# Optimization experiments

Measured on AMD Instinct MI355X. Metric: run time of the kernel, lower is better.

Reference implementation:

```python
import jax, jax.numpy as jnp
import numpy as np

B, T, I, H = 64, 1024, 512, 1024

def setup_inputs() -> dict:
    key = jax.random.key(0)
    k1, k2, k3 = jax.random.split(key, 3)
    x = jax.random.normal(k1, (B, T, I), dtype=jnp.float32)
    # xavier_uniform for input_w, orthogonal for hidden_w (approx: QR of gaussian)
    limit = float(np.sqrt(6.0 / (I + H)))
    input_w = jax.random.uniform(k2, (I, H), minval=-limit, maxval=limit, dtype=jnp.float32)
    g = jax.random.normal(k3, (H, H), dtype=jnp.float32)
    q, r = jnp.linalg.qr(g)
    hidden_w = q * jnp.sign(jnp.diag(r))[None, :]
    b = jnp.zeros((H,), dtype=jnp.float32)
    return {"x": x, "hidden_w": hidden_w, "input_w": input_w, "b": b}

def reference(x, hidden_w, input_w, b):
    # Precompute input projection in one batched GEMM: [B,T,H]
    xp = jnp.einsum('bti,ih->bth', x, input_w) + b
    h0 = jnp.zeros((x.shape[0], hidden_w.shape[0]), dtype=x.dtype)

    def step(h, xt):  # xt: [B,H]
        h = jnp.tanh(h @ hidden_w + xt)
        return h, h

    _, hs = jax.lax.scan(step, h0, jnp.swapaxes(xp, 0, 1))  # hs: [T,B,H]
    return jnp.swapaxes(hs, 0, 1)  # [B,T,H]
```

## Files before the change

kernel.cpp:

```cpp
#include <hip/hip_runtime.h>

#define B_  64
#define T_  1024
#define I_  512
#define H_  1024

typedef short short8 __attribute__((ext_vector_type(8)));
typedef float f32x4  __attribute__((ext_vector_type(4)));
typedef unsigned int u32x4 __attribute__((ext_vector_type(4)));
typedef unsigned long long u64;

__device__ __forceinline__ unsigned short f2bf(float f) {
    unsigned int u = __float_as_uint(f);
    unsigned int r = u + 0x7fffu + ((u >> 16) & 1u);
    return (unsigned short)(r >> 16);
}
__device__ __forceinline__ float bf2f(unsigned short s) {
    return __uint_as_float(((unsigned int)s) << 16);
}

__device__ __forceinline__ u32x4 load_b128_agent(const void* p) {
    u32x4 r;
    asm volatile("global_load_dwordx4 %0, %1, off sc1"
                 : "=v"(r) : "v"(p) : "memory");
    return r;
}

#define BM 128
#define BN 128
#define BK 8

__global__ __launch_bounds__(256) void proj_kernel(
    const float* __restrict__ x, const float* __restrict__ w,
    const float* __restrict__ bias, float* __restrict__ out)
{
    __shared__ float As[BK][BM];
    __shared__ float Bs[BK][BN];

    const int tid = threadIdx.x;
    const int m0 = blockIdx.y * BM;
    const int n0 = blockIdx.x * BN;
    const int tx = tid & 15;
    const int ty = tid >> 4;

    const int arow = tid >> 1;
    const int acol = (tid & 1) * 4;
    const int brow = tid >> 5;
    const int bcol = (tid & 31) * 4;

    float acc[2][4][2][4];
    #pragma unroll
    for (int a = 0; a < 2; a++)
        #pragma unroll
        for (int b = 0; b < 4; b++)
            #pragma unroll
            for (int c = 0; c < 2; c++)
                #pragma unroll
                for (int d = 0; d < 4; d++) acc[a][b][c][d] = 0.f;

    for (int k0 = 0; k0 < I_; k0 += BK) {
        float4 av = *(const float4*)&x[(size_t)(m0 + arow) * I_ + k0 + acol];
        float4 bv = *(const float4*)&w[(size_t)(k0 + brow) * H_ + n0 + bcol];
        __syncthreads();
        As[acol + 0][arow] = av.x;
        As[acol + 1][arow] = av.y;
        As[acol + 2][arow] = av.z;
        As[acol + 3][arow] = av.w;
        *(float4*)&Bs[brow][bcol] = bv;
        __syncthreads();
        #pragma unroll
        for (int kk = 0; kk < BK; kk++) {
            float4 a0 = *(const float4*)&As[kk][ty * 4];
            float4 a1 = *(const float4*)&As[kk][64 + ty * 4];
            float4 b0 = *(const float4*)&Bs[kk][tx * 4];
            float4 b1 = *(const float4*)&Bs[kk][64 + tx * 4];
            const float am[2][4] = {{a0.x,a0.y,a0.z,a0.w},{a1.x,a1.y,a1.z,a1.w}};
            const float bn[2][4] = {{b0.x,b0.y,b0.z,b0.w},{b1.x,b1.y,b1.z,b1.w}};
            #pragma unroll
            for (int mb = 0; mb < 2; mb++)
                #pragma unroll
                for (int mr = 0; mr < 4; mr++)
                    #pragma unroll
                    for (int nb = 0; nb < 2; nb++)
                        #pragma unroll
                        for (int nr = 0; nr < 4; nr++)
                            acc[mb][mr][nb][nr] += am[mb][mr] * bn[nb][nr];
        }
    }

    float4 bias0 = *(const float4*)&bias[n0 + tx * 4];
    float4 bias1 = *(const float4*)&bias[n0 + 64 + tx * 4];
    const float bb[2][4] = {{bias0.x,bias0.y,bias0.z,bias0.w},
                            {bias1.x,bias1.y,bias1.z,bias1.w}};
    #pragma unroll
    for (int mb = 0; mb < 2; mb++)
        #pragma unroll
        for (int mr = 0; mr < 4; mr++) {
            int m = m0 + mb * 64 + ty * 4 + mr;
            #pragma unroll
            for (int nb = 0; nb < 2; nb++) {
                float4 v;
                v.x = acc[mb][mr][nb][0] + bb[nb][0];
                v.y = acc[mb][mr][nb][1] + bb[nb][1];
                v.z = acc[mb][mr][nb][2] + bb[nb][2];
                v.w = acc[mb][mr][nb][3] + bb[nb][3];
                *(float4*)&out[(size_t)m * H_ + n0 + nb * 64 + tx * 4] = v;
            }
        }
}

#define PFD 8

__global__ __launch_bounds__(256, 1) void scan_kernel(
    const float* __restrict__ W,
    float* __restrict__ out,
    unsigned int* __restrict__ hbuf,
    int* __restrict__ flags)
{
    __shared__ short8 wlds[32][64];

    const int wg   = blockIdx.x;
    const int tid  = threadIdx.x;
    const int wave = tid >> 6;
    const int lane = tid & 63;
    const int quad = lane >> 4;
    const int l16  = lane & 15;
    const int jbase = wg * 16;
    const int b0    = wave * 16;
    const int j     = jbase + l16;

    short8 wh[32];
    #pragma unroll
    for (int kc = 0; kc < 32; kc++) {
        short8 wlv;
        #pragma unroll
        for (int i = 0; i < 8; i++) {
            float wv = W[(size_t)(kc * 32 + quad * 8 + i) * H_ + j];
            unsigned short hi = f2bf(wv);
            wh[kc][i] = (short)hi;
            wlv[i] = (short)f2bf(wv - bf2f(hi));
        }
        if ((kc >> 3) == wave) wlds[kc][lane] = wlv;
    }
    __syncthreads();

    const size_t TH = (size_t)T_ * H_;
    size_t oidx[4];
    float xv[4];
    #pragma unroll
    for (int r = 0; r < 4; r++) {
        int b = b0 + quad * 4 + r;
        oidx[r] = (size_t)b * TH + j;
        xv[r] = out[oidx[r]];
    }

    const char* hb_base = (const char*)hbuf + (size_t)wave * 65536
                        + (size_t)lane * 16;
    const int pbase = ((j >> 5) << 9) + (((j >> 2) & 1) << 8)
                    + ((j >> 3) & 3) * 64 + quad * 16 + (j & 3);
    unsigned int* pb_base = hbuf + (size_t)wave * 16384 + pbase;

    int* flagp = flags + wave * 64;

    for (int t = 0; t < T_; t++) {
        float nxv[4] = {0.f, 0.f, 0.f, 0.f};
        if (t + 1 < T_) {
            #pragma unroll
            for (int r = 0; r < 4; r++) nxv[r] = out[oidx[r] + H_];
        }

        f32x4 a0 = {0.f,0.f,0.f,0.f}, a1 = {0.f,0.f,0.f,0.f},
              a2 = {0.f,0.f,0.f,0.f};
        if (t > 0) {
            while (true) {
                int v = __hip_atomic_load(&flagp[lane], __ATOMIC_RELAXED,
                                          __HIP_MEMORY_SCOPE_AGENT);
                if (__all(v >= t)) break;
            }
            __builtin_amdgcn_fence(__ATOMIC_ACQUIRE, "workgroup");

            const char* hb = hb_base + (size_t)((t - 1) & 1) * 262144;

            u32x4 buf[PFD][2];
            #pragma unroll
            for (int d = 0; d < PFD; d++) {
                buf[d][0] = load_b128_agent(hb + d * 2048);
                buf[d][1] = load_b128_agent(hb + d * 2048 + 1024);
            }

            #pragma unroll
            for (int kc = 0; kc < 32; kc++) {
                if (kc < 24) {
                    asm volatile("s_waitcnt vmcnt(14)" ::: "memory");
                } else if (kc == 24) {
                    asm volatile("s_waitcnt vmcnt(0)" ::: "memory");
                }
                __builtin_amdgcn_sched_barrier(0);

                u32x4 c0 = buf[kc & (PFD - 1)][0];
                u32x4 c1 = buf[kc & (PFD - 1)][1];
                short8 ah, al;
                #pragma unroll
                for (int i = 0; i < 4; i++) {
                    ah[i]     = (short)(c0[i] >> 16);
                    al[i]     = (short)(c0[i] & 0xffffu);
                    ah[4 + i] = (short)(c1[i] >> 16);
                    al[4 + i] = (short)(c1[i] & 0xffffu);
                }
                short8 wlv = wlds[kc][lane];
                a0 = __builtin_amdgcn_mfma_f32_16x16x32_bf16(ah, wh[kc], a0, 0, 0, 0);
                a1 = __builtin_amdgcn_mfma_f32_16x16x32_bf16(ah, wlv,    a1, 0, 0, 0);
                a2 = __builtin_amdgcn_mfma_f32_16x16x32_bf16(al, wh[kc], a2, 0, 0, 0);

                if (kc + PFD < 32) {
                    buf[kc & (PFD - 1)][0] =
                        load_b128_agent(hb + (kc + PFD) * 2048);
                    buf[kc & (PFD - 1)][1] =
                        load_b128_agent(hb + (kc + PFD) * 2048 + 1024);
                }
            }
        }

        float hv[4];
        #pragma unroll
        for (int r = 0; r < 4; r++)
            hv[r] = tanhf(a0[r] + a1[r] + a2[r] + xv[r]);

        if (t + 1 < T_) {
            unsigned int* pb = pb_base + (size_t)(t & 1) * 65536;
            #pragma unroll
            for (int r = 0; r < 4; r++) {
                unsigned short hi = f2bf(hv[r]);
                unsigned short lo = f2bf(hv[r] - bf2f(hi));
                unsigned int pk = ((unsigned int)hi << 16) | (unsigned int)lo;
                __hip_atomic_store(&pb[r * 4], pk, __ATOMIC_RELAXED,
                                   __HIP_MEMORY_SCOPE_AGENT);
            }
            asm volatile("s_waitcnt vmcnt(0)" ::: "memory");
            if (lane == 0)
                __hip_atomic_store(&flagp[wg], t + 1, __ATOMIC_RELAXED,
                                   __HIP_MEMORY_SCOPE_AGENT);
        }

        #pragma unroll
        for (int r = 0; r < 4; r++) {
            out[oidx[r]] = hv[r];
            oidx[r] += H_;
            xv[r] = nxv[r];
        }
    }
}

extern "C" void kernel_launch(void* const* d_in, const int* in_sizes, int n_in,
                              void* d_out, int out_size, void* d_ws, size_t ws_size,
                              hipStream_t stream) {
    const float* x        = (const float*)d_in[0];
    const float* hidden_w = (const float*)d_in[1];
    const float* input_w  = (const float*)d_in[2];
    const float* bias     = (const float*)d_in[3];
    float* out = (float*)d_out;

    unsigned int* hbuf = (unsigned int*)d_ws;
    int* flags = (int*)((char*)d_ws + (size_t)512 * 1024);

    hipMemsetAsync(flags, 0, 4 * 64 * sizeof(int), stream);

    dim3 pgrid(H_ / BN, (B_ * T_) / BM);
    proj_kernel<<<pgrid, 256, 0, stream>>>(x, input_w, bias, out);
    scan_kernel<<<64, 256, 0, stream>>>(hidden_w, out, hbuf, flags);
}
```

Measured before the change: 8.276 ms.

## Halve scan workgroups to 32, each computing 32 hidden columns from LDS weights

The persistent scan kernel now runs 32 workgroups instead of 64, and each one computes two 16-column groups of the hidden state per step. Both the high and low bf16 weight splits now sit in LDS instead of the high split being held in registers. Fewer workgroups means fewer flags to poll in the per-step grid-wide barrier, and a short sleep is added to the spin loop. The cost is twice the MFMA work per workgroup on the serial critical path, plus extra LDS reads each step.

```diff
diff --git a/kernel.cpp b/kernel.cpp
--- a/kernel.cpp
+++ b/kernel.cpp
@@ -110,6 +110,7 @@
 }
 
 #define PFD 8
+#define NWG 32
 
 __global__ __launch_bounds__(256, 1) void scan_kernel(
     const float* __restrict__ W,
@@ -117,7 +118,8 @@
     unsigned int* __restrict__ hbuf,
     int* __restrict__ flags)
 {
-    __shared__ short8 wlds[32][64];
+    __shared__ short8 whds[2][32][64];
+    __shared__ short8 wlds[2][32][64];
 
     const int wg   = blockIdx.x;
     const int tid  = threadIdx.x;
@@ -125,57 +127,78 @@
     const int lane = tid & 63;
     const int quad = lane >> 4;
     const int l16  = lane & 15;
-    const int jbase = wg * 16;
+    const int jbase = wg * 32;
     const int b0    = wave * 16;
-    const int j     = jbase + l16;
-
-    short8 wh[32];
+
     #pragma unroll
     for (int kc = 0; kc < 32; kc++) {
-        short8 wlv;
-        #pragma unroll
-        for (int i = 0; i < 8; i++) {
-            float wv = W[(size_t)(kc * 32 + quad * 8 + i) * H_ + j];
-            unsigned short hi = f2bf(wv);
-            wh[kc][i] = (short)hi;
-            wlv[i] = (short)f2bf(wv - bf2f(hi));
-        }
-        if ((kc >> 3) == wave) wlds[kc][lane] = wlv;
+        if ((kc >> 3) == wave) {
+            #pragma unroll
+            for (int g = 0; g < 2; g++) {
+                const int j = jbase + g * 16 + l16;
+                short8 whv, wlv;
+                #pragma unroll
+                for (int i = 0; i < 8; i++) {
+                    float wv = W[(size_t)(kc * 32 + quad * 8 + i) * H_ + j];
+                    unsigned short hi = f2bf(wv);
+                    whv[i] = (short)hi;
+                    wlv[i] = (short)f2bf(wv - bf2f(hi));
+                }
+                whds[g][kc][lane] = whv;
+                wlds[g][kc][lane] = wlv;
+            }
+        }
     }
     __syncthreads();
 
     const size_t TH = (size_t)T_ * H_;
     size_t oidx[4];
-    float xv[4];
+    float xv[2][4];
     #pragma unroll
     for (int r = 0; r < 4; r++) {
         int b = b0 + quad * 4 + r;
-        oidx[r] = (size_t)b * TH + j;
-        xv[r] = out[oidx[r]];
+        oidx[r] = (size_t)b * TH + jbase + l16;
+        xv[0][r] = out[oidx[r]];
+        xv[1][r] = out[oidx[r] + 16];
     }
 
     const char* hb_base = (const char*)hbuf + (size_t)wave * 65536
                         + (size_t)lane * 16;
-    const int pbase = ((j >> 5) << 9) + (((j >> 2) & 1) << 8)
-                    + ((j >> 3) & 3) * 64 + quad * 16 + (j & 3);
-    unsigned int* pb_base = hbuf + (size_t)wave * 16384 + pbase;
-
-    int* flagp = flags + wave * 64;
+    unsigned int* pb_base[2];
+    #pragma unroll
+    for (int g = 0; g < 2; g++) {
+        const int pj = jbase + g * 16 + l16;
+        const int pbase = ((pj >> 5) << 9) + (((pj >> 2) & 1) << 8)
+                        + ((pj >> 3) & 3) * 64 + quad * 16 + (pj & 3);
+        pb_base[g] = hbuf + (size_t)wave * 16384 + pbase;
+    }
+
+    int* flagp = flags + wave * NWG;
 
     for (int t = 0; t < T_; t++) {
-        float nxv[4] = {0.f, 0.f, 0.f, 0.f};
+        float nxv[2][4] = {{0.f,0.f,0.f,0.f},{0.f,0.f,0.f,0.f}};
         if (t + 1 < T_) {
             #pragma unroll
-            for (int r = 0; r < 4; r++) nxv[r] = out[oidx[r] + H_];
-        }
-
-        f32x4 a0 = {0.f,0.f,0.f,0.f}, a1 = {0.f,0.f,0.f,0.f},
-              a2 = {0.f,0.f,0.f,0.f};
+            for (int r = 0; r < 4; r++) {
+                nxv[0][r] = out[oidx[r] + H_];
+                nxv[1][r] = out[oidx[r] + H_ + 16];
+            }
+        }
+
+        f32x4 acc[2][3];
+        #pragma unroll
+        for (int g = 0; g < 2; g++)
+            #pragma unroll
+            for (int s = 0; s < 3; s++)
+                acc[g][s] = (f32x4){0.f, 0.f, 0.f, 0.f};
+
         if (t > 0) {
             while (true) {
-                int v = __hip_atomic_load(&flagp[lane], __ATOMIC_RELAXED,
+                int v = __hip_atomic_load(&flagp[lane & (NWG - 1)],
+                                          __ATOMIC_RELAXED,
                                           __HIP_MEMORY_SCOPE_AGENT);
                 if (__all(v >= t)) break;
+                __builtin_amdgcn_s_sleep(1);
             }
             __builtin_amdgcn_fence(__ATOMIC_ACQUIRE, "workgroup");
 
@@ -207,10 +230,16 @@
                     ah[4 + i] = (short)(c1[i] >> 16);
                     al[4 + i] = (short)(c1[i] & 0xffffu);
                 }
-                short8 wlv = wlds[kc][lane];
-                a0 = __builtin_amdgcn_mfma_f32_16x16x32_bf16(ah, wh[kc], a0, 0, 0, 0);
-                a1 = __builtin_amdgcn_mfma_f32_16x16x32_bf16(ah, wlv,    a1, 0, 0, 0);
-                a2 = __builtin_amdgcn_mfma_f32_16x16x32_bf16(al, wh[kc], a2, 0, 0, 0);
+                short8 wh0 = whds[0][kc][lane];
+                short8 wl0 = wlds[0][kc][lane];
+                short8 wh1 = whds[1][kc][lane];
+                short8 wl1 = wlds[1][kc][lane];
+                acc[0][0] = __builtin_amdgcn_mfma_f32_16x16x32_bf16(ah, wh0, acc[0][0], 0, 0, 0);
+                acc[0][1] = __builtin_amdgcn_mfma_f32_16x16x32_bf16(ah, wl0, acc[0][1], 0, 0, 0);
+                acc[0][2] = __builtin_amdgcn_mfma_f32_16x16x32_bf16(al, wh0, acc[0][2], 0, 0, 0);
+                acc[1][0] = __builtin_amdgcn_mfma_f32_16x16x32_bf16(ah, wh1, acc[1][0], 0, 0, 0);
+                acc[1][1] = __builtin_amdgcn_mfma_f32_16x16x32_bf16(ah, wl1, acc[1][1], 0, 0, 0);
+                acc[1][2] = __builtin_amdgcn_mfma_f32_16x16x32_bf16(al, wh1, acc[1][2], 0, 0, 0);
 
                 if (kc + PFD < 32) {
                     buf[kc & (PFD - 1)][0] =
@@ -221,20 +250,27 @@
             }
         }
 
-        float hv[4];
-        #pragma unroll
-        for (int r = 0; r < 4; r++)
-            hv[r] = tanhf(a0[r] + a1[r] + a2[r] + xv[r]);
+        float hv[2][4];
+        #pragma unroll
+        for (int g = 0; g < 2; g++)
+            #pragma unroll
+            for (int r = 0; r < 4; r++)
+                hv[g][r] = tanhf(acc[g][0][r] + acc[g][1][r] + acc[g][2][r]
+                                 + xv[g][r]);
 
         if (t + 1 < T_) {
-            unsigned int* pb = pb_base + (size_t)(t & 1) * 65536;
-            #pragma unroll
-            for (int r = 0; r < 4; r++) {
-                unsigned short hi = f2bf(hv[r]);
-                unsigned short lo = f2bf(hv[r] - bf2f(hi));
-                unsigned int pk = ((unsigned int)hi << 16) | (unsigned int)lo;
-                __hip_atomic_store(&pb[r * 4], pk, __ATOMIC_RELAXED,
-                                   __HIP_MEMORY_SCOPE_AGENT);
+            #pragma unroll
+            for (int g = 0; g < 2; g++) {
+                unsigned int* pb = pb_base[g] + (size_t)(t & 1) * 65536;
+                #pragma unroll
+                for (int r = 0; r < 4; r++) {
+                    unsigned short hi = f2bf(hv[g][r]);
+                    unsigned short lo = f2bf(hv[g][r] - bf2f(hi));
+                    unsigned int pk = ((unsigned int)hi << 16)
+                                    | (unsigned int)lo;
+                    __hip_atomic_store(&pb[r * 4], pk, __ATOMIC_RELAXED,
+                                       __HIP_MEMORY_SCOPE_AGENT);
+                }
             }
             asm volatile("s_waitcnt vmcnt(0)" ::: "memory");
             if (lane == 0)
@@ -244,9 +280,11 @@
 
         #pragma unroll
         for (int r = 0; r < 4; r++) {
-            out[oidx[r]] = hv[r];
+            out[oidx[r]]      = hv[0][r];
+            out[oidx[r] + 16] = hv[1][r];
             oidx[r] += H_;
-            xv[r] = nxv[r];
+            xv[0][r] = nxv[0][r];
+            xv[1][r] = nxv[1][r];
         }
     }
 }
@@ -263,9 +301,9 @@
     unsigned int* hbuf = (unsigned int*)d_ws;
     int* flags = (int*)((char*)d_ws + (size_t)512 * 1024);
 
-    hipMemsetAsync(flags, 0, 4 * 64 * sizeof(int), stream);
+    hipMemsetAsync(flags, 0, 4 * NWG * sizeof(int), stream);
 
     dim3 pgrid(H_ / BN, (B_ * T_) / BM);
     proj_kernel<<<pgrid, 256, 0, stream>>>(x, input_w, bias, out);
-    scan_kernel<<<64, 256, 0, stream>>>(hidden_w, out, hbuf, flags);
-}
+    scan_kernel<<<NWG, 256, 0, stream>>>(hidden_w, out, hbuf, flags);
+}
```

Result: faster. 7.931 ms (-4.2%).
